# Optimization experiments

Hardware: AMD Instinct MI355X
Metric: run time of the kernel (lower is better)

Reference implementation:

```python
import jax, jax.numpy as jnp
import numpy as np

N_NODES = 100000
N_EDGES = 1600000
NFEAT = 128
NHID = 64


def setup_inputs() -> dict:
    key = jax.random.key(0)
    k1, k2, k3, k4 = jax.random.split(key, 4)
    x = jax.random.normal(k1, (N_NODES, NFEAT), dtype=jnp.float32)
    edge_index = jax.random.randint(k2, (2, N_EDGES), 0, N_NODES, dtype=jnp.int64)
    # Glorot-ish scaled weights
    W1 = jax.random.normal(k3, (NFEAT, NHID), dtype=jnp.float32) * (1.0 / np.sqrt(NFEAT))
    b1 = jnp.zeros((NHID,), dtype=jnp.float32)
    W2 = jax.random.normal(k4, (NHID, NFEAT), dtype=jnp.float32) * (1.0 / np.sqrt(NHID))
    b2 = jnp.zeros((NFEAT,), dtype=jnp.float32)
    return {"x": x, "edge_index": edge_index, "W1": W1, "b1": b1, "W2": W2, "b2": b2}


def _gcn_norm(edge_index, num_nodes):
    # PyG GCNConv default: add self-loops, symmetric normalization D^-1/2 A D^-1/2
    src, dst = edge_index[0], edge_index[1]
    loops = jnp.arange(num_nodes, dtype=src.dtype)
    src = jnp.concatenate([src, loops])
    dst = jnp.concatenate([dst, loops])
    ones = jnp.ones(src.shape[0], dtype=jnp.float32)
    deg = jax.ops.segment_sum(ones, dst, num_segments=num_nodes)  # in-degree incl. self-loop
    dinv = jax.lax.rsqrt(deg)  # deg >= 1 due to self-loops
    norm = dinv[src] * dinv[dst]  # [E + N]
    return src, dst, norm


def _gcn_conv(h, W, b, src, dst, norm, num_nodes):
    h = h @ W                                  # [N, d_out] transform first (d_out small)
    msg = norm[:, None] * h[src]               # gather over edges [E+N, d_out]
    out = jax.ops.segment_sum(msg, dst, num_segments=num_nodes)  # scatter-add
    return out + b


def reference(x, edge_index, W1, b1, W2, b2):
    num_nodes = x.shape[0]
    src, dst, norm = _gcn_norm(edge_index, num_nodes)
    h = jax.nn.relu(_gcn_conv(x, W1, b1, src, dst, norm, num_nodes))
    # dropout is identity in eval mode (deterministic reference baseline)
    out = _gcn_conv(h, W2, b2, src, dst, norm, num_nodes)
    return out
```

## Files before the change

### kernel.cpp

```cpp
#include <hip/hip_runtime.h>
#include <hip/hip_fp16.h>

#define NFEAT 128
#define NHID 64
#define MAXB 1024
#define BSHIFT 8
#define BNODES 256
#define PBLK 512
#define DBINS 512

typedef _Float16 f16x8 __attribute__((ext_vector_type(8)));
typedef float f32x4 __attribute__((ext_vector_type(4)));


__device__ __forceinline__ int edge_idx(const int* __restrict__ ei, int is64,
                                        long long E, long long e, int which) {
    long long pos = which ? (E + e) : e;
    return is64 ? ei[2 * pos] : ei[pos];
}

__device__ __forceinline__ void load8(const int* __restrict__ ei, int is64,
                                      long long E, long long e0, int which,
                                      int (&v)[8]) {
    if (is64) {
        const int* base = ei + 2 * (which ? E + e0 : e0);
        int4 a = *(const int4*)(base + 0);
        int4 b = *(const int4*)(base + 4);
        int4 c = *(const int4*)(base + 8);
        int4 d = *(const int4*)(base + 12);
        v[0] = a.x; v[1] = a.z; v[2] = b.x; v[3] = b.z;
        v[4] = c.x; v[5] = c.z; v[6] = d.x; v[7] = d.z;
    } else {
        const int* base = ei + (which ? E + e0 : e0);
        int4 a = *(const int4*)(base + 0);
        int4 b = *(const int4*)(base + 4);
        v[0] = a.x; v[1] = a.y; v[2] = a.z; v[3] = a.w;
        v[4] = b.x; v[5] = b.y; v[6] = b.z; v[7] = b.w;
    }
}

__device__ __forceinline__ int block_is64(const int* __restrict__ ei, int* smem) {
    if (threadIdx.x == 0) smem[0] = 0;
    __syncthreads();
    int acc = 0;
    for (int i = 1 + 2 * (int)threadIdx.x; i < 4096; i += 512)
        acc |= ei[i];
    atomicOr(&smem[0], acc);
    __syncthreads();
    int r = (smem[0] == 0) ? 1 : 0;
    __syncthreads();
    return r;
}

__global__ __launch_bounds__(256) void k_hist(const int* __restrict__ ei, long long E,
                                              long long perblk,
                                              int* __restrict__ blockhist, int NB) {
    __shared__ int smem[1024];
    int is64 = block_is64(ei, smem);
    int* hist = smem;
    for (int i = threadIdx.x; i < NB; i += 256) hist[i] = 0;
    __syncthreads();
    long long lo = (long long)blockIdx.x * perblk;
    long long hi = lo + perblk; if (hi > E) hi = E;
    if (lo < hi) {
        for (long long e0 = lo + (long long)threadIdx.x * 8; e0 + 8 <= hi; e0 += 256 * 8) {
            int d[8];
            load8(ei, is64, E, e0, 1, d);
#pragma unroll
            for (int j = 0; j < 8; ++j)
                atomicAdd(&hist[d[j] >> BSHIFT], 1);
        }
        long long tail = lo + ((hi - lo) & ~7LL);
        for (long long e = tail + threadIdx.x; e < hi; e += 256) {
            int d = edge_idx(ei, is64, E, e, 1);
            atomicAdd(&hist[d >> BSHIFT], 1);
        }
    }
    __syncthreads();
    int* bh = blockhist + (size_t)blockIdx.x * MAXB;
    for (int i = threadIdx.x; i < NB; i += 256) bh[i] = hist[i];
}

__global__ __launch_bounds__(256) void k_colscan(int* __restrict__ blockhist,
                                                 int* __restrict__ gbhist,
                                                 int* __restrict__ deghist,
                                                 int* __restrict__ dcur, int NB) {
    __shared__ int s[256];
    int b = blockIdx.x;
    int t = threadIdx.x;
    if (b < NB) {
        int v0 = blockhist[(size_t)(2 * t) * MAXB + b];
        int v1 = blockhist[(size_t)(2 * t + 1) * MAXB + b];
        int sum = v0 + v1;
        s[t] = sum;
        __syncthreads();
        for (int d = 1; d < 256; d <<= 1) {
            int val = (t >= d) ? s[t - d] : 0;
            __syncthreads();
            s[t] += val;
            __syncthreads();
        }
        int run = s[t] - sum;
        blockhist[(size_t)(2 * t) * MAXB + b] = run;
        blockhist[(size_t)(2 * t + 1) * MAXB + b] = run + v0;
        if (t == 255) gbhist[b] = s[255];
    } else {
        int idx = (b - NB) * 256 + t;
        if (idx < DBINS)            deghist[idx] = 0;
        else if (idx < 2 * DBINS)   dcur[idx - DBINS] = 0;
    }
}

__global__ __launch_bounds__(256) void k_partition(const int* __restrict__ ei, long long E,
                                                   long long perblk,
                                                   const int* __restrict__ gbhist,
                                                   const int* __restrict__ blockhist,
                                                   unsigned* __restrict__ staging, int NB,
                                                   int* __restrict__ boff,
                                                   int* __restrict__ offN) {
    __shared__ int smem[1024];
    __shared__ int s[256];
    int is64 = block_is64(ei, smem);
    int t = threadIdx.x;
    int v[4]; int sum = 0;
#pragma unroll
    for (int j = 0; j < 4; ++j) {
        int i = t * 4 + j;
        v[j] = (i < NB) ? gbhist[i] : 0;
        sum += v[j];
    }
    s[t] = sum;
    __syncthreads();
    for (int d = 1; d < 256; d <<= 1) {
        int val = (t >= d) ? s[t - d] : 0;
        __syncthreads();
        s[t] += val;
        __syncthreads();
    }
    int run = s[t] - sum;
    int* cur = smem;
    const int* bh = blockhist + (size_t)blockIdx.x * MAXB;
    bool b0 = (blockIdx.x == 0);
#pragma unroll
    for (int j = 0; j < 4; ++j) {
        int i = t * 4 + j;
        if (i < NB) cur[i] = run + bh[i];
        if (b0 && i <= NB) boff[i] = run;
        run += v[j];
    }
    if (b0 && t == 255) *offN = s[255];
    __syncthreads();
    long long lo = (long long)blockIdx.x * perblk;
    long long hi = lo + perblk; if (hi > E) hi = E;
    if (lo < hi) {
        for (long long e0 = lo + (long long)threadIdx.x * 8; e0 + 8 <= hi; e0 += 256 * 8) {
            int sv[8], d[8];
            load8(ei, is64, E, e0, 0, sv);
            load8(ei, is64, E, e0, 1, d);
#pragma unroll
            for (int j = 0; j < 8; ++j) {
                int pos = atomicAdd(&cur[d[j] >> BSHIFT], 1);
                staging[pos] = (unsigned)sv[j] | ((unsigned)(d[j] & (BNODES - 1)) << 24);
            }
        }
        long long tail = lo + ((hi - lo) & ~7LL);
        for (long long e = tail + threadIdx.x; e < hi; e += 256) {
            int sv = edge_idx(ei, is64, E, e, 0);
            int d = edge_idx(ei, is64, E, e, 1);
            int pos = atomicAdd(&cur[d >> BSHIFT], 1);
            staging[pos] = (unsigned)sv | ((unsigned)(d & (BNODES - 1)) << 24);
        }
    }
}

__global__ __launch_bounds__(256) void k_bucket(const unsigned* __restrict__ staging,
                                                const int* __restrict__ boff,
                                                int N, int NB,
                                                int* __restrict__ off,
                                                int* __restrict__ esrc,
                                                float* __restrict__ dinv,
                                                int* __restrict__ deghist) {
    __shared__ int cnt_s[BNODES];
    __shared__ int scan_s[BNODES];
    __shared__ int dh[DBINS];
    int t = threadIdx.x;
    for (int b = blockIdx.x; b < NB; b += gridDim.x) {
        int base = b << BSHIFT;
        cnt_s[t] = 0;
        dh[t] = 0; dh[t + 256] = 0;
        __syncthreads();
        int lo = boff[b], hi = boff[b + 1];
        for (int e = lo + t; e < hi; e += 256)
            atomicAdd(&cnt_s[staging[e] >> 24], 1);
        __syncthreads();
        int v = cnt_s[t];
        scan_s[t] = v;
        __syncthreads();
        for (int d = 1; d < 256; d <<= 1) {
            int val = (t >= d) ? scan_s[t - d] : 0;
            __syncthreads();
            scan_s[t] += val;
            __syncthreads();
        }
        int excl = scan_s[t] - v;
        int node = base + t;
        if (node < N) {
            off[node] = lo + excl;
            dinv[node] = rsqrtf((float)v + 1.0f);
            atomicAdd(&dh[v < (DBINS - 1) ? v : (DBINS - 1)], 1);
        }
        __syncthreads();
        if (dh[t])       atomicAdd(&deghist[t], dh[t]);
        if (dh[t + 256]) atomicAdd(&deghist[t + 256], dh[t + 256]);
        cnt_s[t] = lo + excl;
        __syncthreads();
        for (int e = lo + t; e < hi; e += 256) {
            unsigned sd = staging[e];
            int pos = atomicAdd(&cnt_s[sd >> 24], 1);
            esrc[pos] = (int)(sd & 0xFFFFFFu);
        }
        __syncthreads();
    }
}

__global__ __launch_bounds__(256) void k_dperm(const int* __restrict__ off,
                                               const int* __restrict__ deghist,
                                               int* __restrict__ dcur,
                                               int* __restrict__ perm, int N) {
    __shared__ int dbase[DBINS];
    __shared__ int cnt[DBINS];
    __shared__ int base[DBINS];
    __shared__ int s[256];
    int t = threadIdx.x;
    int v0 = deghist[2 * t], v1 = deghist[2 * t + 1];
    int sum = v0 + v1;
    s[t] = sum;
    cnt[t] = 0; cnt[t + 256] = 0;
    __syncthreads();
    for (int d = 1; d < 256; d <<= 1) {
        int val = (t >= d) ? s[t - d] : 0;
        __syncthreads();
        s[t] += val;
        __syncthreads();
    }
    int run = s[t] - sum;
    dbase[2 * t] = run;
    dbase[2 * t + 1] = run + v0;
    __syncthreads();
    int n = blockIdx.x * 256 + t;
    int b = 0, myidx = 0;
    if (n < N) {
        int deg = off[n + 1] - off[n];
        b = deg < (DBINS - 1) ? deg : (DBINS - 1);
        myidx = atomicAdd(&cnt[b], 1);
    }
    __syncthreads();
    int c0 = cnt[t];       if (c0) base[t] = dbase[t] + atomicAdd(&dcur[t], c0);
    int c1 = cnt[t + 256]; if (c1) base[t + 256] = dbase[t + 256] + atomicAdd(&dcur[t + 256], c1);
    __syncthreads();
    if (n < N) perm[base[b] + myidx] = n;
}

__device__ __forceinline__ int swz(int row, int byteoff) {
    return (row << 8) + (byteoff ^ ((row & 7) << 4));
}
__device__ __forceinline__ int swz64(int row, int byteoff) {
    return (row << 7) + (byteoff ^ ((row & 7) << 4));
}

__global__ __launch_bounds__(256) void k_gemm1(const float* __restrict__ x,
                                               const float* __restrict__ W1,
                                               const float* __restrict__ dinv,
                                               __half* __restrict__ xw1s, int N) {
    __shared__ __align__(16) __half xs[64 * NFEAT];
    __shared__ __align__(16) __half ws[NHID * NFEAT];
    int t = threadIdx.x;
    for (int i = t; i < NFEAT * NHID; i += 256) {
        int k = i >> 6, n = i & 63;
        *(__half*)((char*)ws + swz(n, k * 2)) = __float2half(W1[i]);
    }
    int row0 = blockIdx.x * 64;
    for (int i = t; i < 64 * 32; i += 256) {
        int r = i >> 5, c4 = i & 31;
        int row = row0 + r;
        float4 v = (row < N) ? ((const float4*)x)[(size_t)row * 32 + c4]
                             : make_float4(0.f, 0.f, 0.f, 0.f);
        __half2 h0 = __floats2half2_rn(v.x, v.y);
        __half2 h1 = __floats2half2_rn(v.z, v.w);
        uint2 p = make_uint2(*(unsigned*)&h0, *(unsigned*)&h1);
        *(uint2*)((char*)xs + swz(r, c4 * 8)) = p;
    }
    __syncthreads();
    int wave = t >> 6, lane = t & 63;
    int lr = lane & 15, g = lane >> 4;
    int xrow = wave * 16 + lr;
    f16x8 xb[4];
#pragma unroll
    for (int kc = 0; kc < 4; ++kc)
        xb[kc] = *(const f16x8*)((const char*)xs + swz(xrow, kc * 64 + g * 16));
    int row = row0 + xrow;
    float di = (row < N) ? dinv[row] : 0.f;
#pragma unroll
    for (int c = 0; c < 4; ++c) {
        f32x4 acc = {0.f, 0.f, 0.f, 0.f};
#pragma unroll
        for (int kc = 0; kc < 4; ++kc) {
            f16x8 a = *(const f16x8*)((const char*)ws + swz(c * 16 + lr, kc * 64 + g * 16));
            acc = __builtin_amdgcn_mfma_f32_16x16x32_f16(a, xb[kc], acc, 0, 0, 0);
        }
        if (row < N) {
            __half2 o0 = __floats2half2_rn(di * acc[0], di * acc[1]);
            __half2 o1 = __floats2half2_rn(di * acc[2], di * acc[3]);
            uint2 p = make_uint2(*(unsigned*)&o0, *(unsigned*)&o1);
            *(uint2*)&xw1s[(size_t)row * NHID + c * 16 + g * 4] = p;
        }
    }
}

__device__ __forceinline__ void addhalf8(float2 (&acc)[4], uint4 p) {
    const __half2* hh = (const __half2*)&p;
#pragma unroll
    for (int j = 0; j < 4; ++j) {
        float2 v = __half22float2(hh[j]);
        acc[j].x += v.x; acc[j].y += v.y;
    }
}

__device__ __forceinline__ void gather_group(const int* __restrict__ off,
                                             const int* __restrict__ esrc,
                                             const uint4* __restrict__ feat4,
                                             int d, int li, int lo, int hi,
                                             float2 (&acc)[4]) {
#pragma unroll
    for (int j = 0; j < 4; ++j) acc[j] = make_float2(0.f, 0.f);
    int idx = (lo + li < hi) ? esrc[lo + li] : 0;
    for (int e = lo; e < hi; e += 8) {
        int nrem = hi - e;
        int cur = idx;
        int ne = e + 8;
        idx = (ne + li < hi) ? esrc[ne + li] : 0;
        if (nrem >= 8) {
#pragma unroll
            for (int j = 0; j < 8; ++j) {
                int s = __shfl(cur, j, 8);
                addhalf8(acc, feat4[(size_t)s * 8 + li]);
            }
        } else {
            for (int j = 0; j < nrem; ++j) {
                int s = __shfl(cur, j, 8);
                addhalf8(acc, feat4[(size_t)s * 8 + li]);
            }
        }
    }
    addhalf8(acc, feat4[(size_t)d * 8 + li]);
}

__global__ __launch_bounds__(256) void k_agg1(const int* __restrict__ off,
                                              const int* __restrict__ esrc,
                                              const int* __restrict__ perm,
                                              const float* __restrict__ dinv,
                                              const uint4* __restrict__ xw1s4,
                                              const float* __restrict__ b1,
                                              uint4* __restrict__ h4, int N) {
    int t = threadIdx.x;
    int lane = t & 63, wave = t >> 6;
    int g = lane >> 3, li = lane & 7;
    int slot = blockIdx.x * 32 + wave * 8 + g;
    bool valid = slot < N;
    int d  = valid ? perm[slot] : 0;
    int lo = valid ? off[d] : 0;
    int hi = valid ? off[d + 1] : 0;
    float2 acc[4];
    gather_group(off, esrc, xw1s4, d, li, lo, hi, acc);
    float dd = dinv[d];
    float4 bA = ((const float4*)b1)[li * 2 + 0];
    float4 bB = ((const float4*)b1)[li * 2 + 1];
    float v0 = fmaxf(dd * acc[0].x + bA.x, 0.f);
    float v1 = fmaxf(dd * acc[0].y + bA.y, 0.f);
    float v2 = fmaxf(dd * acc[1].x + bA.z, 0.f);
    float v3 = fmaxf(dd * acc[1].y + bA.w, 0.f);
    float v4 = fmaxf(dd * acc[2].x + bB.x, 0.f);
    float v5 = fmaxf(dd * acc[2].y + bB.y, 0.f);
    float v6 = fmaxf(dd * acc[3].x + bB.z, 0.f);
    float v7 = fmaxf(dd * acc[3].y + bB.w, 0.f);
    __half2 o[4];
    o[0] = __floats2half2_rn(dd * v0, dd * v1);
    o[1] = __floats2half2_rn(dd * v2, dd * v3);
    o[2] = __floats2half2_rn(dd * v4, dd * v5);
    o[3] = __floats2half2_rn(dd * v6, dd * v7);
    if (valid) h4[(size_t)d * 8 + li] = *(const uint4*)o;
}

__global__ __launch_bounds__(256) void k_agg2(const int* __restrict__ off,
                                              const int* __restrict__ esrc,
                                              const int* __restrict__ perm,
                                              const float* __restrict__ dinv,
                                              const uint4* __restrict__ h4,
                                              uint4* __restrict__ a2h,
                                              uint4* __restrict__ a2l, int N) {
    int t = threadIdx.x;
    int lane = t & 63, wave = t >> 6;
    int g = lane >> 3, li = lane & 7;
    int slot = blockIdx.x * 32 + wave * 8 + g;
    bool valid = slot < N;
    int d  = valid ? perm[slot] : 0;
    int lo = valid ? off[d] : 0;
    int hi = valid ? off[d + 1] : 0;
    float2 acc[4];
    gather_group(off, esrc, h4, d, li, lo, hi, acc);
    float dd = dinv[d];
    float v[8] = {dd * acc[0].x, dd * acc[0].y, dd * acc[1].x, dd * acc[1].y,
                  dd * acc[2].x, dd * acc[2].y, dd * acc[3].x, dd * acc[3].y};
    __half hh[8], ll[8];
#pragma unroll
    for (int j = 0; j < 8; ++j) {
        hh[j] = __float2half(v[j]);
        ll[j] = __float2half(v[j] - __half2float(hh[j]));
    }
    uint4 ph, pl;
    __half2* hp = (__half2*)&ph;
    __half2* lp = (__half2*)&pl;
#pragma unroll
    for (int j = 0; j < 4; ++j) {
        hp[j] = __halves2half2(hh[2 * j], hh[2 * j + 1]);
        lp[j] = __halves2half2(ll[2 * j], ll[2 * j + 1]);
    }
    if (valid) {
        a2h[(size_t)d * 8 + li] = ph;
        a2l[(size_t)d * 8 + li] = pl;
    }
}

__global__ __launch_bounds__(256) void k_gemm2(const __half* __restrict__ a2h,
                                               const __half* __restrict__ a2l,
                                               const float* __restrict__ W2,
                                               const float* __restrict__ b2,
                                               float* __restrict__ out, int N) {
    __shared__ __align__(16) __half sB[NFEAT * NHID];
    __shared__ __align__(16) __half sH[64 * NHID];
    __shared__ __align__(16) __half sL[64 * NHID];
    int t = threadIdx.x;
    for (int i = t; i < NFEAT * NHID; i += 256) {
        int k = i >> 7, n = i & 127;
        *(__half*)((char*)sB + swz64(n, k * 2)) = __float2half(W2[i]);
    }
    int row0 = blockIdx.x * 64;
    for (int i = t; i < 64 * 8; i += 256) {
        int r = i >> 3, c16 = (i & 7) << 4;
        int row = row0 + r;
        uint4 vh = make_uint4(0, 0, 0, 0), vl = make_uint4(0, 0, 0, 0);
        if (row < N) {
            vh = *(const uint4*)((const char*)a2h + (size_t)row * 128 + c16);
            vl = *(const uint4*)((const char*)a2l + (size_t)row * 128 + c16);
        }
        *(uint4*)((char*)sH + swz64(r, c16)) = vh;
        *(uint4*)((char*)sL + swz64(r, c16)) = vl;
    }
    __syncthreads();
    int wave = t >> 6, lane = t & 63;
    int lr = lane & 15, g = lane >> 4;
    int xrow = wave * 16 + lr;
    f16x8 xh[2], xl[2];
#pragma unroll
    for (int kc = 0; kc < 2; ++kc) {
        xh[kc] = *(const f16x8*)((const char*)sH + swz64(xrow, kc * 64 + g * 16));
        xl[kc] = *(const f16x8*)((const char*)sL + swz64(xrow, kc * 64 + g * 16));
    }
    int row = row0 + xrow;
#pragma unroll
    for (int c = 0; c < 8; ++c) {
        f32x4 acc = {0.f, 0.f, 0.f, 0.f};
#pragma unroll
        for (int kc = 0; kc < 2; ++kc) {
            f16x8 a = *(const f16x8*)((const char*)sB + swz64(c * 16 + lr, kc * 64 + g * 16));
            acc = __builtin_amdgcn_mfma_f32_16x16x32_f16(a, xl[kc], acc, 0, 0, 0);
            acc = __builtin_amdgcn_mfma_f32_16x16x32_f16(a, xh[kc], acc, 0, 0, 0);
        }
        if (row < N) {
            float4 bb = *(const float4*)&b2[c * 16 + g * 4];
            float4 o = make_float4(acc[0] + bb.x, acc[1] + bb.y,
                                   acc[2] + bb.z, acc[3] + bb.w);
            *(float4*)&out[(size_t)row * NFEAT + c * 16 + g * 4] = o;
        }
    }
}

static inline char* align256(char* p) {
    return (char*)(((uintptr_t)p + 255) & ~(uintptr_t)255);
}

extern "C" void kernel_launch(void* const* d_in, const int* in_sizes, int n_in,
                              void* d_out, int out_size, void* d_ws, size_t ws_size,
                              hipStream_t stream) {
    const float* x  = (const float*)d_in[0];
    const int*   ei = (const int*)d_in[1];
    const float* W1 = (const float*)d_in[2];
    const float* b1 = (const float*)d_in[3];
    const float* W2 = (const float*)d_in[4];
    const float* b2 = (const float*)d_in[5];
    float* out = (float*)d_out;

    const int N = in_sizes[0] / NFEAT;
    const long long E = in_sizes[1] / 2;
    const int NB = (N + BNODES - 1) >> BSHIFT;

    char* w = (char*)d_ws;
    int*      gbhist    = (int*)w;
    int*      boff      = gbhist + MAXB;
    int*      deghist   = boff + MAXB + 1;
    int*      dcur      = deghist + DBINS;
    int*      blockhist = dcur + DBINS;
    float*    dinv      = (float*)(blockhist + (size_t)PBLK * MAXB);
    int*      off       = (int*)(dinv + N);
    int*      perm      = off + N + 1;
    char*     p         = align256((char*)(perm + N));
    unsigned* staging   = (unsigned*)p;
    p = align256((char*)(staging + E));
    int*      esrc      = (int*)p;
    p = align256((char*)(esrc + E));
    __half*   xw1s      = (__half*)p;
    p = align256((char*)(xw1s + (size_t)N * NHID));
    __half*   h         = (__half*)p;
    p = align256((char*)(h + (size_t)N * NHID));
    __half*   a2h       = (__half*)p;
    p = align256((char*)(a2h + (size_t)N * NHID));
    __half*   a2l       = (__half*)p;

    long long perblk = ((E + PBLK - 1) / PBLK + 7) & ~7LL;

    k_hist<<<PBLK, 256, 0, stream>>>(ei, E, perblk, blockhist, NB);
    k_colscan<<<NB + 4, 256, 0, stream>>>(blockhist, gbhist, deghist, dcur, NB);
    k_partition<<<PBLK, 256, 0, stream>>>(ei, E, perblk, gbhist, blockhist, staging,
                                          NB, boff, off + N);
    k_bucket<<<NB, 256, 0, stream>>>(staging, boff, N, NB, off, esrc, dinv, deghist);
    k_dperm<<<(N + 255) / 256, 256, 0, stream>>>(off, deghist, dcur, perm, N);

    k_gemm1<<<(N + 63) / 64, 256, 0, stream>>>(x, W1, dinv, xw1s, N);

    k_agg1<<<(N + 31) / 32, 256, 0, stream>>>(off, esrc, perm, dinv, (const uint4*)xw1s,
                                              b1, (uint4*)h, N);
    k_agg2<<<(N + 31) / 32, 256, 0, stream>>>(off, esrc, perm, dinv, (const uint4*)h,
                                              (uint4*)a2h, (uint4*)a2l, N);

    k_gemm2<<<(N + 63) / 64, 256, 0, stream>>>(a2h, a2l, W2, b2, out, N);
}
```

Before: 266.5 us.

## Fuse second-layer aggregation with the W2 GEMM in one kernel

Merges the layer-2 gather/aggregate kernel with the following W2 GEMM. Each 32-node block writes its aggregated hi/lo fp16 rows into shared memory, then does the MFMA product and stores output rows scattered by permuted node id. This drops the a2h/a2l round trip through global memory and one launch. In exchange, every block reloads and converts the whole W2 into shared memory for only 32 rows, output writes become scattered by perm, and the larger shared-memory footprint may lower occupancy of the gather phase.

```diff
diff --git a/kernel.cpp b/kernel.cpp
--- a/kernel.cpp
+++ b/kernel.cpp
@@ -391,17 +391,27 @@
     if (valid) h4[(size_t)d * 8 + li] = *(const uint4*)o;
 }
 
-__global__ __launch_bounds__(256) void k_agg2(const int* __restrict__ off,
-                                              const int* __restrict__ esrc,
-                                              const int* __restrict__ perm,
-                                              const float* __restrict__ dinv,
-                                              const uint4* __restrict__ h4,
-                                              uint4* __restrict__ a2h,
-                                              uint4* __restrict__ a2l, int N) {
-    int t = threadIdx.x;
+__global__ __launch_bounds__(256) void k_agg2g2(const int* __restrict__ off,
+                                                const int* __restrict__ esrc,
+                                                const int* __restrict__ perm,
+                                                const float* __restrict__ dinv,
+                                                const uint4* __restrict__ h4,
+                                                const float* __restrict__ W2,
+                                                const float* __restrict__ b2,
+                                                float* __restrict__ out, int N) {
+    __shared__ __align__(16) __half sB[NFEAT * NHID];
+    __shared__ __align__(16) __half sH[32 * NHID];
+    __shared__ __align__(16) __half sL[32 * NHID];
+    __shared__ int nid[32];
+    int t = threadIdx.x;
+    for (int i = t; i < NFEAT * NHID; i += 256) {
+        int k = i >> 7, n = i & 127;
+        *(__half*)((char*)sB + swz64(n, k * 2)) = __float2half(W2[i]);
+    }
     int lane = t & 63, wave = t >> 6;
     int g = lane >> 3, li = lane & 7;
-    int slot = blockIdx.x * 32 + wave * 8 + g;
+    int gi = wave * 8 + g;
+    int slot = blockIdx.x * 32 + gi;
     bool valid = slot < N;
     int d  = valid ? perm[slot] : 0;
     int lo = valid ? off[d] : 0;
@@ -425,62 +435,35 @@
         hp[j] = __halves2half2(hh[2 * j], hh[2 * j + 1]);
         lp[j] = __halves2half2(ll[2 * j], ll[2 * j + 1]);
     }
-    if (valid) {
-        a2h[(size_t)d * 8 + li] = ph;
-        a2l[(size_t)d * 8 + li] = pl;
-    }
-}
-
-__global__ __launch_bounds__(256) void k_gemm2(const __half* __restrict__ a2h,
-                                               const __half* __restrict__ a2l,
-                                               const float* __restrict__ W2,
-                                               const float* __restrict__ b2,
-                                               float* __restrict__ out, int N) {
-    __shared__ __align__(16) __half sB[NFEAT * NHID];
-    __shared__ __align__(16) __half sH[64 * NHID];
-    __shared__ __align__(16) __half sL[64 * NHID];
-    int t = threadIdx.x;
-    for (int i = t; i < NFEAT * NHID; i += 256) {
-        int k = i >> 7, n = i & 127;
-        *(__half*)((char*)sB + swz64(n, k * 2)) = __float2half(W2[i]);
-    }
-    int row0 = blockIdx.x * 64;
-    for (int i = t; i < 64 * 8; i += 256) {
-        int r = i >> 3, c16 = (i & 7) << 4;
-        int row = row0 + r;
-        uint4 vh = make_uint4(0, 0, 0, 0), vl = make_uint4(0, 0, 0, 0);
-        if (row < N) {
-            vh = *(const uint4*)((const char*)a2h + (size_t)row * 128 + c16);
-            vl = *(const uint4*)((const char*)a2l + (size_t)row * 128 + c16);
-        }
-        *(uint4*)((char*)sH + swz64(r, c16)) = vh;
-        *(uint4*)((char*)sL + swz64(r, c16)) = vl;
-    }
-    __syncthreads();
-    int wave = t >> 6, lane = t & 63;
-    int lr = lane & 15, g = lane >> 4;
-    int xrow = wave * 16 + lr;
+    *(uint4*)((char*)sH + swz64(gi, li * 16)) = ph;
+    *(uint4*)((char*)sL + swz64(gi, li * 16)) = pl;
+    if (li == 0) nid[gi] = valid ? d : -1;
+    __syncthreads();
+    int lr = lane & 15, g2 = lane >> 4;
+    int rtile = wave & 1, chalf = wave >> 1;
+    int xrow = rtile * 16 + lr;
+    int node = nid[xrow];
     f16x8 xh[2], xl[2];
 #pragma unroll
     for (int kc = 0; kc < 2; ++kc) {
-        xh[kc] = *(const f16x8*)((const char*)sH + swz64(xrow, kc * 64 + g * 16));
-        xl[kc] = *(const f16x8*)((const char*)sL + swz64(xrow, kc * 64 + g * 16));
-    }
-    int row = row0 + xrow;
-#pragma unroll
-    for (int c = 0; c < 8; ++c) {
-        f32x4 acc = {0.f, 0.f, 0.f, 0.f};
+        xh[kc] = *(const f16x8*)((const char*)sH + swz64(xrow, kc * 64 + g2 * 16));
+        xl[kc] = *(const f16x8*)((const char*)sL + swz64(xrow, kc * 64 + g2 * 16));
+    }
+#pragma unroll
+    for (int ci = 0; ci < 4; ++ci) {
+        int c = chalf * 4 + ci;
+        f32x4 a2 = {0.f, 0.f, 0.f, 0.f};
 #pragma unroll
         for (int kc = 0; kc < 2; ++kc) {
-            f16x8 a = *(const f16x8*)((const char*)sB + swz64(c * 16 + lr, kc * 64 + g * 16));
-            acc = __builtin_amdgcn_mfma_f32_16x16x32_f16(a, xl[kc], acc, 0, 0, 0);
-            acc = __builtin_amdgcn_mfma_f32_16x16x32_f16(a, xh[kc], acc, 0, 0, 0);
-        }
-        if (row < N) {
-            float4 bb = *(const float4*)&b2[c * 16 + g * 4];
-            float4 o = make_float4(acc[0] + bb.x, acc[1] + bb.y,
-                                   acc[2] + bb.z, acc[3] + bb.w);
-            *(float4*)&out[(size_t)row * NFEAT + c * 16 + g * 4] = o;
+            f16x8 a = *(const f16x8*)((const char*)sB + swz64(c * 16 + lr, kc * 64 + g2 * 16));
+            a2 = __builtin_amdgcn_mfma_f32_16x16x32_f16(a, xl[kc], a2, 0, 0, 0);
+            a2 = __builtin_amdgcn_mfma_f32_16x16x32_f16(a, xh[kc], a2, 0, 0, 0);
+        }
+        if (node >= 0) {
+            float4 bb = *(const float4*)&b2[c * 16 + g2 * 4];
+            float4 o = make_float4(a2[0] + bb.x, a2[1] + bb.y,
+                                   a2[2] + bb.z, a2[3] + bb.w);
+            *(float4*)&out[(size_t)node * NFEAT + c * 16 + g2 * 4] = o;
         }
     }
 }
@@ -521,10 +504,6 @@
     __half*   xw1s      = (__half*)p;
     p = align256((char*)(xw1s + (size_t)N * NHID));
     __half*   h         = (__half*)p;
-    p = align256((char*)(h + (size_t)N * NHID));
-    __half*   a2h       = (__half*)p;
-    p = align256((char*)(a2h + (size_t)N * NHID));
-    __half*   a2l       = (__half*)p;
 
     long long perblk = ((E + PBLK - 1) / PBLK + 7) & ~7LL;
 
@@ -539,8 +518,6 @@
 
     k_agg1<<<(N + 31) / 32, 256, 0, stream>>>(off, esrc, perm, dinv, (const uint4*)xw1s,
                                               b1, (uint4*)h, N);
-    k_agg2<<<(N + 31) / 32, 256, 0, stream>>>(off, esrc, perm, dinv, (const uint4*)h,
-                                              (uint4*)a2h, (uint4*)a2l, N);
-
-    k_gemm2<<<(N + 63) / 64, 256, 0, stream>>>(a2h, a2l, W2, b2, out, N);
-}
+    k_agg2g2<<<(N + 31) / 32, 256, 0, stream>>>(off, esrc, perm, dinv, (const uint4*)h,
+                                                W2, b2, out, N);
+}
```

After: 260.5 us. 1.02x faster.
